# Performance work log

Measured on AMD Instinct MI355X. Metric: run time of the kernel, lower is better.

The kernel has to match this reference:

```python
import jax, jax.numpy as jnp
import numpy as np

N_GROUPS = 368
NMODELS = 64
BATCH = 4096


def setup_inputs() -> dict:
    key = jax.random.key(0)
    kx, kw, kb = jax.random.split(key, 3)
    x = jax.random.normal(kx, (BATCH, N_GROUPS, NMODELS), dtype=jnp.float32)
    # torch.nn.Linear default init: U(-1/sqrt(fan_in), 1/sqrt(fan_in))
    bound = 1.0 / np.sqrt(NMODELS)
    # W[i] is the [out, in] weight of the i-th Linear
    W = jax.random.uniform(kw, (N_GROUPS, NMODELS, NMODELS), dtype=jnp.float32, minval=-bound, maxval=bound)
    b = jax.random.uniform(kb, (N_GROUPS, NMODELS), dtype=jnp.float32, minval=-bound, maxval=bound)
    return {"x": x, "W": W, "b": b}


def reference(x, W, b):
    # y[b,g,:] = x[b,g,:] @ W[g].T + b[g]  -> grouped tiny GEMM, batched as one einsum
    y = jnp.einsum('bgn,gmn->bgm', x, W) + b[None, :, :]
    resp = jax.nn.softmax(y, axis=-1)  # softmax over feature axis per group
    # elementwise mul with x and reduce feature axis -> [B, 368]
    return (resp * x).sum(axis=-1)
```

## Files before the change

kernel.cpp:

```cpp
#include <hip/hip_runtime.h>
#include <hip/hip_bf16.h>

#define N_GROUPS 368
#define NMODELS  64
#define BATCH    4096
#define ROWS     256

typedef __attribute__((ext_vector_type(8)))  short short8v;
typedef __attribute__((ext_vector_type(16))) float f32x16;

__device__ inline void bf_split(float v, unsigned short& hi, unsigned short& lo) {
    const __hip_bfloat16 h = __float2bfloat16(v);
    const float r = v - __bfloat162float(h);
    const __hip_bfloat16 l = __float2bfloat16(r);
    hi = __builtin_bit_cast(unsigned short, h);
    lo = __builtin_bit_cast(unsigned short, l);
}

__device__ inline float bf2f(short u) {
    return __builtin_bit_cast(float, ((unsigned)(unsigned short)u) << 16);
}

#define SWZ(row, soff) ((soff) ^ (((row) & 7) << 3))

__global__ __launch_bounds__(512, 4) void ensemble_mfma_t(
    const float* __restrict__ x,
    const float* __restrict__ W,
    const float* __restrict__ bias,
    float* __restrict__ out)
{
    __shared__ __hip_bfloat16 Xh[ROWS * 64];
    __shared__ __hip_bfloat16 Xl[ROWS * 64];
    __shared__ __hip_bfloat16 Wh[64 * 64];
    __shared__ __hip_bfloat16 Wl[64 * 64];

    const int g    = blockIdx.y;
    const int row0 = blockIdx.x * ROWS;
    const int t    = threadIdx.x;
    const int q    = t >> 4;
    const int ui   = t & 15;

    #pragma unroll
    for (int j = 0; j < 8; ++j) {
        const int r = q + 32 * j;
        const float4 v = *reinterpret_cast<const float4*>(
            x + ((size_t)(row0 + r) * N_GROUPS + g) * NMODELS + 4 * ui);
        unsigned short h0,h1,h2_,h3, l0,l1,l2,l3;
        bf_split(v.x, h0, l0); bf_split(v.y, h1, l1);
        bf_split(v.z, h2_, l2); bf_split(v.w, h3, l3);
        const int so = r * 64 + SWZ(r, 4 * ui);
        *reinterpret_cast<short4*>(&Xh[so]) = make_short4((short)h0,(short)h1,(short)h2_,(short)h3);
        *reinterpret_cast<short4*>(&Xl[so]) = make_short4((short)l0,(short)l1,(short)l2,(short)l3);
    }
    #pragma unroll
    for (int j = 0; j < 2; ++j) {
        const int m = q + 32 * j;
        const float4 v = *reinterpret_cast<const float4*>(
            W + ((size_t)g * 64 + m) * 64 + 4 * ui);
        unsigned short h0,h1,h2_,h3, l0,l1,l2,l3;
        bf_split(v.x, h0, l0); bf_split(v.y, h1, l1);
        bf_split(v.z, h2_, l2); bf_split(v.w, h3, l3);
        const int so = m * 64 + SWZ(m, 4 * ui);
        *reinterpret_cast<short4*>(&Wh[so]) = make_short4((short)h0,(short)h1,(short)h2_,(short)h3);
        *reinterpret_cast<short4*>(&Wl[so]) = make_short4((short)l0,(short)l1,(short)l2,(short)l3);
    }

    const int lane = t & 63;
    const int wv   = t >> 6;
    const int cl   = lane & 31;
    const int h2   = lane >> 5;

    __syncthreads();

    f32x16 acc0, acc1;
    #pragma unroll
    for (int r = 0; r < 16; ++r) { acc0[r] = 0.f; acc1[r] = 0.f; }

    const int c = wv * 32 + cl;
    #pragma unroll
    for (int ks = 0; ks < 4; ++ks) {
        const int ko = ks * 16 + 8 * h2;
        const int xo = c * 64 + SWZ(c, ko);
        const short8v bh = *reinterpret_cast<const short8v*>(&Xh[xo]);
        const short8v bl = *reinterpret_cast<const short8v*>(&Xl[xo]);

        const int wo0 = cl * 64 + SWZ(cl, ko);
        const short8v ah0 = *reinterpret_cast<const short8v*>(&Wh[wo0]);
        const short8v al0 = *reinterpret_cast<const short8v*>(&Wl[wo0]);
        acc0 = __builtin_amdgcn_mfma_f32_32x32x16_bf16(ah0, bh, acc0, 0, 0, 0);
        acc0 = __builtin_amdgcn_mfma_f32_32x32x16_bf16(ah0, bl, acc0, 0, 0, 0);
        acc0 = __builtin_amdgcn_mfma_f32_32x32x16_bf16(al0, bh, acc0, 0, 0, 0);

        const int m1  = 32 + cl;
        const int wo1 = m1 * 64 + SWZ(m1, ko);
        const short8v ah1 = *reinterpret_cast<const short8v*>(&Wh[wo1]);
        const short8v al1 = *reinterpret_cast<const short8v*>(&Wl[wo1]);
        acc1 = __builtin_amdgcn_mfma_f32_32x32x16_bf16(ah1, bh, acc1, 0, 0, 0);
        acc1 = __builtin_amdgcn_mfma_f32_32x32x16_bf16(ah1, bl, acc1, 0, 0, 0);
        acc1 = __builtin_amdgcn_mfma_f32_32x32x16_bf16(al1, bh, acc1, 0, 0, 0);
    }

    float4 bv4[2][4];
    #pragma unroll
    for (int tt = 0; tt < 2; ++tt)
        #pragma unroll
        for (int rq = 0; rq < 4; ++rq)
            bv4[tt][rq] = *reinterpret_cast<const float4*>(
                bias + (size_t)g * 64 + tt * 32 + 8 * rq + 4 * h2);

    float y[2][16];
    #pragma unroll
    for (int tt = 0; tt < 2; ++tt)
        #pragma unroll
        for (int rq = 0; rq < 4; ++rq) {
            const f32x16& a = tt ? acc1 : acc0;
            y[tt][4*rq+0] = a[4*rq+0] + bv4[tt][rq].x;
            y[tt][4*rq+1] = a[4*rq+1] + bv4[tt][rq].y;
            y[tt][4*rq+2] = a[4*rq+2] + bv4[tt][rq].z;
            y[tt][4*rq+3] = a[4*rq+3] + bv4[tt][rq].w;
        }

    float mx = y[0][0];
    #pragma unroll
    for (int r = 1; r < 16; ++r) mx = fmaxf(mx, y[0][r]);
    #pragma unroll
    for (int r = 0; r < 16; ++r) mx = fmaxf(mx, y[1][r]);
    mx = fmaxf(mx, __shfl_xor(mx, 32));

    float S = 0.f, P = 0.f;
    #pragma unroll
    for (int tt = 0; tt < 2; ++tt)
        #pragma unroll
        for (int j = 0; j < 4; ++j) {
            const int so = c * 64 + SWZ(c, tt * 32 + 8 * j + 4 * h2);
            const short4 vh = *reinterpret_cast<const short4*>(&Xh[so]);
            const short4 vl = *reinterpret_cast<const short4*>(&Xl[so]);
            const float xv0 = bf2f(vh.x) + bf2f(vl.x);
            const float xv1 = bf2f(vh.y) + bf2f(vl.y);
            const float xv2 = bf2f(vh.z) + bf2f(vl.z);
            const float xv3 = bf2f(vh.w) + bf2f(vl.w);
            const float e0 = __expf(y[tt][4*j+0] - mx);
            const float e1 = __expf(y[tt][4*j+1] - mx);
            const float e2 = __expf(y[tt][4*j+2] - mx);
            const float e3 = __expf(y[tt][4*j+3] - mx);
            S += (e0 + e1) + (e2 + e3);
            P = __builtin_fmaf(e0, xv0, P);
            P = __builtin_fmaf(e1, xv1, P);
            P = __builtin_fmaf(e2, xv2, P);
            P = __builtin_fmaf(e3, xv3, P);
        }
    S += __shfl_xor(S, 32);
    P += __shfl_xor(P, 32);

    if (h2 == 0)
        out[(size_t)(row0 + c) * N_GROUPS + g] = P / S;
}

extern "C" void kernel_launch(void* const* d_in, const int* in_sizes, int n_in,
                              void* d_out, int out_size, void* d_ws, size_t ws_size,
                              hipStream_t stream) {
    const float* x  = (const float*)d_in[0];
    const float* W  = (const float*)d_in[1];
    const float* b  = (const float*)d_in[2];
    float* out = (float*)d_out;

    dim3 grid(BATCH / ROWS, N_GROUPS);
    dim3 block(512);
    ensemble_mfma_t<<<grid, block, 0, stream>>>(x, W, b, out);
}
```

Measured before the change: 108.7 us.

## Tile blocks over 8 groups × 32 rows, load W directly into registers

Each block now covers 8 consecutive groups and 32 batch rows instead of one group and 256 rows, with each wave owning one group. The x tile load becomes one contiguous 2 KB span per row rather than 256-byte strided pieces. W is read straight from global memory into registers and split to bf16 hi/lo per wave, so the shared W staging is dropped. The cost is many more blocks, and the W for each group is now re-read by every row-block (128 times instead of 16) and re-split in registers.

```diff
diff --git a/kernel.cpp b/kernel.cpp
--- a/kernel.cpp
+++ b/kernel.cpp
@@ -4,7 +4,8 @@
 #define N_GROUPS 368
 #define NMODELS  64
 #define BATCH    4096
-#define ROWS     256
+#define RPB      32
+#define GPB      8
 
 typedef __attribute__((ext_vector_type(8)))  short short8v;
 typedef __attribute__((ext_vector_type(16))) float f32x16;
@@ -21,80 +22,88 @@
     return __builtin_bit_cast(float, ((unsigned)(unsigned short)u) << 16);
 }
 
+__device__ inline void split8(const float4 a, const float4 b, short8v& h, short8v& l) {
+    unsigned short hh, ll;
+    bf_split(a.x, hh, ll); h[0] = (short)hh; l[0] = (short)ll;
+    bf_split(a.y, hh, ll); h[1] = (short)hh; l[1] = (short)ll;
+    bf_split(a.z, hh, ll); h[2] = (short)hh; l[2] = (short)ll;
+    bf_split(a.w, hh, ll); h[3] = (short)hh; l[3] = (short)ll;
+    bf_split(b.x, hh, ll); h[4] = (short)hh; l[4] = (short)ll;
+    bf_split(b.y, hh, ll); h[5] = (short)hh; l[5] = (short)ll;
+    bf_split(b.z, hh, ll); h[6] = (short)hh; l[6] = (short)ll;
+    bf_split(b.w, hh, ll); h[7] = (short)hh; l[7] = (short)ll;
+}
+
 #define SWZ(row, soff) ((soff) ^ (((row) & 7) << 3))
 
-__global__ __launch_bounds__(512, 4) void ensemble_mfma_t(
+__global__ __launch_bounds__(512, 4) void ensemble_mg(
     const float* __restrict__ x,
     const float* __restrict__ W,
     const float* __restrict__ bias,
     float* __restrict__ out)
 {
-    __shared__ __hip_bfloat16 Xh[ROWS * 64];
-    __shared__ __hip_bfloat16 Xl[ROWS * 64];
-    __shared__ __hip_bfloat16 Wh[64 * 64];
-    __shared__ __hip_bfloat16 Wl[64 * 64];
+    __shared__ __hip_bfloat16 Xh[GPB][RPB * 64];
+    __shared__ __hip_bfloat16 Xl[GPB][RPB * 64];
 
-    const int g    = blockIdx.y;
-    const int row0 = blockIdx.x * ROWS;
+    const int g0   = blockIdx.y * GPB;
+    const int row0 = blockIdx.x * RPB;
     const int t    = threadIdx.x;
-    const int q    = t >> 4;
-    const int ui   = t & 15;
-
-    #pragma unroll
-    for (int j = 0; j < 8; ++j) {
-        const int r = q + 32 * j;
-        const float4 v = *reinterpret_cast<const float4*>(
-            x + ((size_t)(row0 + r) * N_GROUPS + g) * NMODELS + 4 * ui);
-        unsigned short h0,h1,h2_,h3, l0,l1,l2,l3;
-        bf_split(v.x, h0, l0); bf_split(v.y, h1, l1);
-        bf_split(v.z, h2_, l2); bf_split(v.w, h3, l3);
-        const int so = r * 64 + SWZ(r, 4 * ui);
-        *reinterpret_cast<short4*>(&Xh[so]) = make_short4((short)h0,(short)h1,(short)h2_,(short)h3);
-        *reinterpret_cast<short4*>(&Xl[so]) = make_short4((short)l0,(short)l1,(short)l2,(short)l3);
-    }
-    #pragma unroll
-    for (int j = 0; j < 2; ++j) {
-        const int m = q + 32 * j;
-        const float4 v = *reinterpret_cast<const float4*>(
-            W + ((size_t)g * 64 + m) * 64 + 4 * ui);
-        unsigned short h0,h1,h2_,h3, l0,l1,l2,l3;
-        bf_split(v.x, h0, l0); bf_split(v.y, h1, l1);
-        bf_split(v.z, h2_, l2); bf_split(v.w, h3, l3);
-        const int so = m * 64 + SWZ(m, 4 * ui);
-        *reinterpret_cast<short4*>(&Wh[so]) = make_short4((short)h0,(short)h1,(short)h2_,(short)h3);
-        *reinterpret_cast<short4*>(&Wl[so]) = make_short4((short)l0,(short)l1,(short)l2,(short)l3);
-    }
 
     const int lane = t & 63;
     const int wv   = t >> 6;
     const int cl   = lane & 31;
     const int h2   = lane >> 5;
+    const int g    = g0 + wv;
 
+    const float* __restrict__ Wg = W + (size_t)g * NMODELS * NMODELS;
+    float4 wr[4][4];
+    #pragma unroll
+    for (int ks = 0; ks < 4; ++ks) {
+        const int ko = ks * 16 + 8 * h2;
+        wr[ks][0] = *reinterpret_cast<const float4*>(Wg + cl * 64 + ko);
+        wr[ks][1] = *reinterpret_cast<const float4*>(Wg + cl * 64 + ko + 4);
+        wr[ks][2] = *reinterpret_cast<const float4*>(Wg + (32 + cl) * 64 + ko);
+        wr[ks][3] = *reinterpret_cast<const float4*>(Wg + (32 + cl) * 64 + ko + 4);
+    }
+
+    #pragma unroll
+    for (int j = 0; j < 8; ++j) {
+        const int r   = (t >> 7) + 4 * j;
+        const int idx = (t & 127) * 4;
+        const int gi  = idx >> 6;
+        const int n0  = idx & 63;
+        const float4 v = *reinterpret_cast<const float4*>(
+            x + ((size_t)(row0 + r) * N_GROUPS + g0) * NMODELS + idx);
+        unsigned short h_[4], l_[4];
+        bf_split(v.x, h_[0], l_[0]); bf_split(v.y, h_[1], l_[1]);
+        bf_split(v.z, h_[2], l_[2]); bf_split(v.w, h_[3], l_[3]);
+        const int so = r * 64 + SWZ(r, n0);
+        *reinterpret_cast<short4*>(&Xh[gi][so]) =
+            make_short4((short)h_[0], (short)h_[1], (short)h_[2], (short)h_[3]);
+        *reinterpret_cast<short4*>(&Xl[gi][so]) =
+            make_short4((short)l_[0], (short)l_[1], (short)l_[2], (short)l_[3]);
+    }
     __syncthreads();
 
     f32x16 acc0, acc1;
     #pragma unroll
     for (int r = 0; r < 16; ++r) { acc0[r] = 0.f; acc1[r] = 0.f; }
 
-    const int c = wv * 32 + cl;
     #pragma unroll
     for (int ks = 0; ks < 4; ++ks) {
         const int ko = ks * 16 + 8 * h2;
-        const int xo = c * 64 + SWZ(c, ko);
-        const short8v bh = *reinterpret_cast<const short8v*>(&Xh[xo]);
-        const short8v bl = *reinterpret_cast<const short8v*>(&Xl[xo]);
+        const int xo = cl * 64 + SWZ(cl, ko);
+        const short8v bh = *reinterpret_cast<const short8v*>(&Xh[wv][xo]);
+        const short8v bl = *reinterpret_cast<const short8v*>(&Xl[wv][xo]);
 
-        const int wo0 = cl * 64 + SWZ(cl, ko);
-        const short8v ah0 = *reinterpret_cast<const short8v*>(&Wh[wo0]);
-        const short8v al0 = *reinterpret_cast<const short8v*>(&Wl[wo0]);
+        short8v ah0, al0, ah1, al1;
+        split8(wr[ks][0], wr[ks][1], ah0, al0);
+        split8(wr[ks][2], wr[ks][3], ah1, al1);
+
         acc0 = __builtin_amdgcn_mfma_f32_32x32x16_bf16(ah0, bh, acc0, 0, 0, 0);
         acc0 = __builtin_amdgcn_mfma_f32_32x32x16_bf16(ah0, bl, acc0, 0, 0, 0);
         acc0 = __builtin_amdgcn_mfma_f32_32x32x16_bf16(al0, bh, acc0, 0, 0, 0);
 
-        const int m1  = 32 + cl;
-        const int wo1 = m1 * 64 + SWZ(m1, ko);
-        const short8v ah1 = *reinterpret_cast<const short8v*>(&Wh[wo1]);
-        const short8v al1 = *reinterpret_cast<const short8v*>(&Wl[wo1]);
         acc1 = __builtin_amdgcn_mfma_f32_32x32x16_bf16(ah1, bh, acc1, 0, 0, 0);
         acc1 = __builtin_amdgcn_mfma_f32_32x32x16_bf16(ah1, bl, acc1, 0, 0, 0);
         acc1 = __builtin_amdgcn_mfma_f32_32x32x16_bf16(al1, bh, acc1, 0, 0, 0);
@@ -132,9 +141,9 @@
     for (int tt = 0; tt < 2; ++tt)
         #pragma unroll
         for (int j = 0; j < 4; ++j) {
-            const int so = c * 64 + SWZ(c, tt * 32 + 8 * j + 4 * h2);
-            const short4 vh = *reinterpret_cast<const short4*>(&Xh[so]);
-            const short4 vl = *reinterpret_cast<const short4*>(&Xl[so]);
+            const int so = cl * 64 + SWZ(cl, tt * 32 + 8 * j + 4 * h2);
+            const short4 vh = *reinterpret_cast<const short4*>(&Xh[wv][so]);
+            const short4 vl = *reinterpret_cast<const short4*>(&Xl[wv][so]);
             const float xv0 = bf2f(vh.x) + bf2f(vl.x);
             const float xv1 = bf2f(vh.y) + bf2f(vl.y);
             const float xv2 = bf2f(vh.z) + bf2f(vl.z);
@@ -153,7 +162,7 @@
     P += __shfl_xor(P, 32);
 
     if (h2 == 0)
-        out[(size_t)(row0 + c) * N_GROUPS + g] = P / S;
+        out[(size_t)(row0 + cl) * N_GROUPS + g] = P / S;
 }
 
 extern "C" void kernel_launch(void* const* d_in, const int* in_sizes, int n_in,
@@ -164,7 +173,7 @@
     const float* b  = (const float*)d_in[2];
     float* out = (float*)d_out;
 
-    dim3 grid(BATCH / ROWS, N_GROUPS);
+    dim3 grid(BATCH / RPB, N_GROUPS / GPB);
     dim3 block(512);
-    ensemble_mfma_t<<<grid, block, 0, stream>>>(x, W, b, out);
+    ensemble_mg<<<grid, block, 0, stream>>>(x, W, b, out);
 }
```

New measurement: 151.8 us. +39.7%, slower.

## Split x staging into two K-halves overlapping loads with first-half MFMAs

Applied to the files above, without the earlier changes.

Stages the x tile in two halves. The second half of the feature columns is loaded into registers while MFMAs run on the first half, then converted and stored behind a second barrier. The thread-to-data mapping changes so each thread loads 16 contiguous floats of one row, and the bf16 hi/lo split now uses integer rounding bit tricks that pack two values per word. The aim is to hide global load latency and cut conversion instruction count, at the cost of an extra barrier and more live registers.

```diff
diff --git a/kernel.cpp b/kernel.cpp
--- a/kernel.cpp
+++ b/kernel.cpp
@@ -1,5 +1,6 @@
 #include <hip/hip_runtime.h>
 #include <hip/hip_bf16.h>
+#include <stdint.h>
 
 #define N_GROUPS 368
 #define NMODELS  64
@@ -9,21 +10,24 @@
 typedef __attribute__((ext_vector_type(8)))  short short8v;
 typedef __attribute__((ext_vector_type(16))) float f32x16;
 
-__device__ inline void bf_split(float v, unsigned short& hi, unsigned short& lo) {
-    const __hip_bfloat16 h = __float2bfloat16(v);
-    const float r = v - __bfloat162float(h);
-    const __hip_bfloat16 l = __float2bfloat16(r);
-    hi = __builtin_bit_cast(unsigned short, h);
-    lo = __builtin_bit_cast(unsigned short, l);
+__device__ inline uint32_t f2u(float f) { return __builtin_bit_cast(uint32_t, f); }
+__device__ inline float    u2f(uint32_t u) { return __builtin_bit_cast(float, u); }
+__device__ inline float    bf2f(short s) { return u2f(((uint32_t)(unsigned short)s) << 16); }
+
+__device__ inline void split4(const float4 v, uint2& hp, uint2& lp) {
+    const uint32_t hx = (f2u(v.x) + 0x8000u) & 0xFFFF0000u;
+    const uint32_t hy = (f2u(v.y) + 0x8000u) & 0xFFFF0000u;
+    const uint32_t hz = (f2u(v.z) + 0x8000u) & 0xFFFF0000u;
+    const uint32_t hw = (f2u(v.w) + 0x8000u) & 0xFFFF0000u;
+    hp.x = (hx >> 16) | hy;
+    hp.y = (hz >> 16) | hw;
+    lp.x = (f2u(v.x - u2f(hx)) >> 16) | (f2u(v.y - u2f(hy)) & 0xFFFF0000u);
+    lp.y = (f2u(v.z - u2f(hz)) >> 16) | (f2u(v.w - u2f(hw)) & 0xFFFF0000u);
 }
 
-__device__ inline float bf2f(short u) {
-    return __builtin_bit_cast(float, ((unsigned)(unsigned short)u) << 16);
-}
-
 #define SWZ(row, soff) ((soff) ^ (((row) & 7) << 3))
 
-__global__ __launch_bounds__(512, 4) void ensemble_mfma_t(
+__global__ __launch_bounds__(512, 4) void ensemble_pipe(
     const float* __restrict__ x,
     const float* __restrict__ W,
     const float* __restrict__ bias,
@@ -37,48 +41,91 @@
     const int g    = blockIdx.y;
     const int row0 = blockIdx.x * ROWS;
     const int t    = threadIdx.x;
-    const int q    = t >> 4;
-    const int ui   = t & 15;
-
-    #pragma unroll
-    for (int j = 0; j < 8; ++j) {
-        const int r = q + 32 * j;
-        const float4 v = *reinterpret_cast<const float4*>(
-            x + ((size_t)(row0 + r) * N_GROUPS + g) * NMODELS + 4 * ui);
-        unsigned short h0,h1,h2_,h3, l0,l1,l2,l3;
-        bf_split(v.x, h0, l0); bf_split(v.y, h1, l1);
-        bf_split(v.z, h2_, l2); bf_split(v.w, h3, l3);
-        const int so = r * 64 + SWZ(r, 4 * ui);
-        *reinterpret_cast<short4*>(&Xh[so]) = make_short4((short)h0,(short)h1,(short)h2_,(short)h3);
-        *reinterpret_cast<short4*>(&Xl[so]) = make_short4((short)l0,(short)l1,(short)l2,(short)l3);
+
+    const int sr = t >> 1;
+    const int f0 = (t & 1) * 16;
+    const float* __restrict__ xrow =
+        x + ((size_t)(row0 + sr) * N_GROUPS + g) * NMODELS;
+
+    const int wm = t >> 3;
+    const int wc = (t & 7) * 8;
+    const float* __restrict__ Wgp =
+        W + (size_t)g * NMODELS * NMODELS + (size_t)wm * NMODELS + wc;
+
+    float4 q0[4];
+    #pragma unroll
+    for (int j = 0; j < 4; ++j)
+        q0[j] = *reinterpret_cast<const float4*>(xrow + f0 + 4 * j);
+    float4 wq[2];
+    #pragma unroll
+    for (int j = 0; j < 2; ++j)
+        wq[j] = *reinterpret_cast<const float4*>(Wgp + 4 * j);
+
+    #pragma unroll
+    for (int j = 0; j < 4; ++j) {
+        uint2 hp, lp; split4(q0[j], hp, lp);
+        const int so = sr * 64 + SWZ(sr, f0 + 4 * j);
+        *reinterpret_cast<uint2*>(&Xh[so]) = hp;
+        *reinterpret_cast<uint2*>(&Xl[so]) = lp;
     }
     #pragma unroll
     for (int j = 0; j < 2; ++j) {
-        const int m = q + 32 * j;
-        const float4 v = *reinterpret_cast<const float4*>(
-            W + ((size_t)g * 64 + m) * 64 + 4 * ui);
-        unsigned short h0,h1,h2_,h3, l0,l1,l2,l3;
-        bf_split(v.x, h0, l0); bf_split(v.y, h1, l1);
-        bf_split(v.z, h2_, l2); bf_split(v.w, h3, l3);
-        const int so = m * 64 + SWZ(m, 4 * ui);
-        *reinterpret_cast<short4*>(&Wh[so]) = make_short4((short)h0,(short)h1,(short)h2_,(short)h3);
-        *reinterpret_cast<short4*>(&Wl[so]) = make_short4((short)l0,(short)l1,(short)l2,(short)l3);
-    }
+        uint2 hp, lp; split4(wq[j], hp, lp);
+        const int so = wm * 64 + SWZ(wm, wc + 4 * j);
+        *reinterpret_cast<uint2*>(&Wh[so]) = hp;
+        *reinterpret_cast<uint2*>(&Wl[so]) = lp;
+    }
+    __syncthreads();
+
+    float4 q1[4];
+    #pragma unroll
+    for (int j = 0; j < 4; ++j)
+        q1[j] = *reinterpret_cast<const float4*>(xrow + 32 + f0 + 4 * j);
 
     const int lane = t & 63;
     const int wv   = t >> 6;
     const int cl   = lane & 31;
     const int h2   = lane >> 5;
-
+    const int c    = wv * 32 + cl;
+
+    f32x16 acc0, acc1;
+    #pragma unroll
+    for (int r = 0; r < 16; ++r) { acc0[r] = 0.f; acc1[r] = 0.f; }
+
+    #pragma unroll
+    for (int ks = 0; ks < 2; ++ks) {
+        const int ko = ks * 16 + 8 * h2;
+        const int xo = c * 64 + SWZ(c, ko);
+        const short8v bh = *reinterpret_cast<const short8v*>(&Xh[xo]);
+        const short8v bl = *reinterpret_cast<const short8v*>(&Xl[xo]);
+
+        const int wo0 = cl * 64 + SWZ(cl, ko);
+        const short8v ah0 = *reinterpret_cast<const short8v*>(&Wh[wo0]);
+        const short8v al0 = *reinterpret_cast<const short8v*>(&Wl[wo0]);
+        acc0 = __builtin_amdgcn_mfma_f32_32x32x16_bf16(ah0, bh, acc0, 0, 0, 0);
+        acc0 = __builtin_amdgcn_mfma_f32_32x32x16_bf16(ah0, bl, acc0, 0, 0, 0);
+        acc0 = __builtin_amdgcn_mfma_f32_32x32x16_bf16(al0, bh, acc0, 0, 0, 0);
+
+        const int m1  = 32 + cl;
+        const int wo1 = m1 * 64 + SWZ(m1, ko);
+        const short8v ah1 = *reinterpret_cast<const short8v*>(&Wh[wo1]);
+        const short8v al1 = *reinterpret_cast<const short8v*>(&Wl[wo1]);
+        acc1 = __builtin_amdgcn_mfma_f32_32x32x16_bf16(ah1, bh, acc1, 0, 0, 0);
+        acc1 = __builtin_amdgcn_mfma_f32_32x32x16_bf16(ah1, bl, acc1, 0, 0, 0);
+        acc1 = __builtin_amdgcn_mfma_f32_32x32x16_bf16(al1, bh, acc1, 0, 0, 0);
+    }
+
+    #pragma unroll
+    for (int j = 0; j < 4; ++j) {
+        uint2 hp, lp; split4(q1[j], hp, lp);
+        const int so = sr * 64 + SWZ(sr, 32 + f0 + 4 * j);
+        *reinterpret_cast<uint2*>(&Xh[so]) = hp;
+        *reinterpret_cast<uint2*>(&Xl[so]) = lp;
+    }
     __syncthreads();
 
-    f32x16 acc0, acc1;
-    #pragma unroll
-    for (int r = 0; r < 16; ++r) { acc0[r] = 0.f; acc1[r] = 0.f; }
-
-    const int c = wv * 32 + cl;
-    #pragma unroll
-    for (int ks = 0; ks < 4; ++ks) {
+    #pragma unroll
+    for (int ks = 2; ks < 4; ++ks) {
         const int ko = ks * 16 + 8 * h2;
         const int xo = c * 64 + SWZ(c, ko);
         const short8v bh = *reinterpret_cast<const short8v*>(&Xh[xo]);
@@ -166,5 +213,5 @@
 
     dim3 grid(BATCH / ROWS, N_GROUPS);
     dim3 block(512);
-    ensemble_mfma_t<<<grid, block, 0, stream>>>(x, W, b, out);
+    ensemble_pipe<<<grid, block, 0, stream>>>(x, W, b, out);
 }
```

Result: slower. 118.5 us (+9.0%).

## Load x directly into MFMA registers, dropping the x shared-memory staging

Applied to the files above, without the earlier changes.

Each lane now reads its x row fragments straight from global memory and splits them into bf16 hi/lo in registers, instead of staging the whole x tile through LDS. Only W is still staged, so shared memory per block shrinks a lot. Blocks are halved to 256 threads covering 128 rows, and the bf16 split is rewritten with integer rounding bit tricks. The x loads are now per-lane strided 32-byte reads, each row touched by two lanes, and the epilogue re-reads x from global, likely from cache. That may lower coalescing in exchange for higher occupancy and no x staging.

```diff
diff --git a/kernel.cpp b/kernel.cpp
--- a/kernel.cpp
+++ b/kernel.cpp
@@ -1,88 +1,89 @@
 #include <hip/hip_runtime.h>
 #include <hip/hip_bf16.h>
+#include <stdint.h>
 
 #define N_GROUPS 368
 #define NMODELS  64
 #define BATCH    4096
-#define ROWS     256
+#define ROWS     128
 
 typedef __attribute__((ext_vector_type(8)))  short short8v;
 typedef __attribute__((ext_vector_type(16))) float f32x16;
 
-__device__ inline void bf_split(float v, unsigned short& hi, unsigned short& lo) {
-    const __hip_bfloat16 h = __float2bfloat16(v);
-    const float r = v - __bfloat162float(h);
-    const __hip_bfloat16 l = __float2bfloat16(r);
-    hi = __builtin_bit_cast(unsigned short, h);
-    lo = __builtin_bit_cast(unsigned short, l);
+__device__ inline uint32_t f2u(float f) { return __builtin_bit_cast(uint32_t, f); }
+__device__ inline float    u2f(uint32_t u) { return __builtin_bit_cast(float, u); }
+
+__device__ inline void split4(const float4 v, uint2& hp, uint2& lp) {
+    const uint32_t hx = (f2u(v.x) + 0x8000u) & 0xFFFF0000u;
+    const uint32_t hy = (f2u(v.y) + 0x8000u) & 0xFFFF0000u;
+    const uint32_t hz = (f2u(v.z) + 0x8000u) & 0xFFFF0000u;
+    const uint32_t hw = (f2u(v.w) + 0x8000u) & 0xFFFF0000u;
+    hp.x = (hx >> 16) | hy;
+    hp.y = (hz >> 16) | hw;
+    lp.x = (f2u(v.x - u2f(hx)) >> 16) | (f2u(v.y - u2f(hy)) & 0xFFFF0000u);
+    lp.y = (f2u(v.z - u2f(hz)) >> 16) | (f2u(v.w - u2f(hw)) & 0xFFFF0000u);
 }
 
-__device__ inline float bf2f(short u) {
-    return __builtin_bit_cast(float, ((unsigned)(unsigned short)u) << 16);
+__device__ inline void split8(const float4 a, const float4 b, short8v& h, short8v& l) {
+    uint2 ha, la, hb, lb;
+    split4(a, ha, la);
+    split4(b, hb, lb);
+    const uint4 hu = make_uint4(ha.x, ha.y, hb.x, hb.y);
+    const uint4 lu = make_uint4(la.x, la.y, lb.x, lb.y);
+    h = __builtin_bit_cast(short8v, hu);
+    l = __builtin_bit_cast(short8v, lu);
 }
 
 #define SWZ(row, soff) ((soff) ^ (((row) & 7) << 3))
 
-__global__ __launch_bounds__(512, 4) void ensemble_mfma_t(
+__global__ __launch_bounds__(256, 3) void ensemble_nobar(
     const float* __restrict__ x,
     const float* __restrict__ W,
     const float* __restrict__ bias,
     float* __restrict__ out)
 {
-    __shared__ __hip_bfloat16 Xh[ROWS * 64];
-    __shared__ __hip_bfloat16 Xl[ROWS * 64];
     __shared__ __hip_bfloat16 Wh[64 * 64];
     __shared__ __hip_bfloat16 Wl[64 * 64];
 
     const int g    = blockIdx.y;
     const int row0 = blockIdx.x * ROWS;
     const int t    = threadIdx.x;
-    const int q    = t >> 4;
-    const int ui   = t & 15;
 
-    #pragma unroll
-    for (int j = 0; j < 8; ++j) {
-        const int r = q + 32 * j;
-        const float4 v = *reinterpret_cast<const float4*>(
-            x + ((size_t)(row0 + r) * N_GROUPS + g) * NMODELS + 4 * ui);
-        unsigned short h0,h1,h2_,h3, l0,l1,l2,l3;
-        bf_split(v.x, h0, l0); bf_split(v.y, h1, l1);
-        bf_split(v.z, h2_, l2); bf_split(v.w, h3, l3);
-        const int so = r * 64 + SWZ(r, 4 * ui);
-        *reinterpret_cast<short4*>(&Xh[so]) = make_short4((short)h0,(short)h1,(short)h2_,(short)h3);
-        *reinterpret_cast<short4*>(&Xl[so]) = make_short4((short)l0,(short)l1,(short)l2,(short)l3);
+    {
+        const int wm = t >> 2;
+        const int wc = (t & 3) * 16;
+        const float* __restrict__ Wgp =
+            W + (size_t)g * (NMODELS * NMODELS) + (size_t)wm * NMODELS + wc;
+        #pragma unroll
+        for (int j = 0; j < 4; ++j) {
+            const float4 v = *reinterpret_cast<const float4*>(Wgp + 4 * j);
+            uint2 hp, lp; split4(v, hp, lp);
+            const int so = wm * 64 + SWZ(wm, wc + 4 * j);
+            *reinterpret_cast<uint2*>(&Wh[so]) = hp;
+            *reinterpret_cast<uint2*>(&Wl[so]) = lp;
+        }
     }
-    #pragma unroll
-    for (int j = 0; j < 2; ++j) {
-        const int m = q + 32 * j;
-        const float4 v = *reinterpret_cast<const float4*>(
-            W + ((size_t)g * 64 + m) * 64 + 4 * ui);
-        unsigned short h0,h1,h2_,h3, l0,l1,l2,l3;
-        bf_split(v.x, h0, l0); bf_split(v.y, h1, l1);
-        bf_split(v.z, h2_, l2); bf_split(v.w, h3, l3);
-        const int so = m * 64 + SWZ(m, 4 * ui);
-        *reinterpret_cast<short4*>(&Wh[so]) = make_short4((short)h0,(short)h1,(short)h2_,(short)h3);
-        *reinterpret_cast<short4*>(&Wl[so]) = make_short4((short)l0,(short)l1,(short)l2,(short)l3);
-    }
+    __syncthreads();
 
     const int lane = t & 63;
     const int wv   = t >> 6;
     const int cl   = lane & 31;
     const int h2   = lane >> 5;
+    const int c    = wv * 32 + cl;
 
-    __syncthreads();
+    const float* __restrict__ xr =
+        x + ((size_t)(row0 + c) * N_GROUPS + g) * NMODELS;
 
     f32x16 acc0, acc1;
     #pragma unroll
     for (int r = 0; r < 16; ++r) { acc0[r] = 0.f; acc1[r] = 0.f; }
 
-    const int c = wv * 32 + cl;
     #pragma unroll
     for (int ks = 0; ks < 4; ++ks) {
         const int ko = ks * 16 + 8 * h2;
-        const int xo = c * 64 + SWZ(c, ko);
-        const short8v bh = *reinterpret_cast<const short8v*>(&Xh[xo]);
-        const short8v bl = *reinterpret_cast<const short8v*>(&Xl[xo]);
+        const float4 xa = *reinterpret_cast<const float4*>(xr + ko);
+        const float4 xb = *reinterpret_cast<const float4*>(xr + ko + 4);
+        short8v bh, bl; split8(xa, xb, bh, bl);
 
         const int wo0 = cl * 64 + SWZ(cl, ko);
         const short8v ah0 = *reinterpret_cast<const short8v*>(&Wh[wo0]);
@@ -132,22 +133,17 @@
     for (int tt = 0; tt < 2; ++tt)
         #pragma unroll
         for (int j = 0; j < 4; ++j) {
-            const int so = c * 64 + SWZ(c, tt * 32 + 8 * j + 4 * h2);
-            const short4 vh = *reinterpret_cast<const short4*>(&Xh[so]);
-            const short4 vl = *reinterpret_cast<const short4*>(&Xl[so]);
-            const float xv0 = bf2f(vh.x) + bf2f(vl.x);
-            const float xv1 = bf2f(vh.y) + bf2f(vl.y);
-            const float xv2 = bf2f(vh.z) + bf2f(vl.z);
-            const float xv3 = bf2f(vh.w) + bf2f(vl.w);
+            const float4 xv4 = *reinterpret_cast<const float4*>(
+                xr + tt * 32 + 8 * j + 4 * h2);
             const float e0 = __expf(y[tt][4*j+0] - mx);
             const float e1 = __expf(y[tt][4*j+1] - mx);
             const float e2 = __expf(y[tt][4*j+2] - mx);
             const float e3 = __expf(y[tt][4*j+3] - mx);
             S += (e0 + e1) + (e2 + e3);
-            P = __builtin_fmaf(e0, xv0, P);
-            P = __builtin_fmaf(e1, xv1, P);
-            P = __builtin_fmaf(e2, xv2, P);
-            P = __builtin_fmaf(e3, xv3, P);
+            P = __builtin_fmaf(e0, xv4.x, P);
+            P = __builtin_fmaf(e1, xv4.y, P);
+            P = __builtin_fmaf(e2, xv4.z, P);
+            P = __builtin_fmaf(e3, xv4.w, P);
         }
     S += __shfl_xor(S, 32);
     P += __shfl_xor(P, 32);
@@ -165,6 +161,6 @@
     float* out = (float*)d_out;
 
     dim3 grid(BATCH / ROWS, N_GROUPS);
-    dim3 block(512);
-    ensemble_mfma_t<<<grid, block, 0, stream>>>(x, W, b, out);
+    dim3 block(256);
+    ensemble_nobar<<<grid, block, 0, stream>>>(x, W, b, out);
 }
```

Measured after the change: 197.6 us. 1.82x slower.
